# Optimization experiments

Hardware: AMD Instinct MI355X
Metric: run time of the kernel (lower is better)

## Reference

```python
import jax, jax.numpy as jnp
import numpy as np

L = 11
SF = 2
N, C, H, W = 8, 8, 256, 256


def _conv3(x, w, b):
    y = jax.lax.conv_general_dilated(x, w, (1, 1), ((1, 1), (1, 1)),
                                     dimension_numbers=('NCHW', 'OIHW', 'NCHW'))
    return y + b[None, :, None, None]


def _resblock(x, wa, ba, wb, bb):
    return _conv3(jax.nn.relu(_conv3(x, wa, ba)), wb, bb)


def _pronet(g, w1a, b1a, w1b, b1b, w2a, b2a, w2b, b2b, w3a, b3a, w3b, b3b,
            w4a, b4a, w4b, b4b, w5, b5):
    x1 = jax.nn.relu(g + 0.1 * _resblock(g, w1a, b1a, w1b, b1b))
    x2 = jax.nn.relu(x1 + 0.1 * _resblock(x1, w2a, b2a, w2b, b2b))
    x3 = jax.nn.relu(x2 + 0.1 * _resblock(x2, w3a, b3a, w3b, b3b))
    x4 = jax.nn.relu(x3 + 0.1 * _resblock(x3, w4a, b4a, w4b, b4b))
    return jax.nn.relu(g + 0.1 * _conv3(x4, w5, b5))


def _im2col(x, l, sf):
    # reflect-pad by (l-1)//2 then extract l x l patches with stride sf
    # -> [N, C, l*l, h*w], matching torch unfold's (c, kh, kw) channel order
    pad = (l - 1) // 2
    xp = jnp.pad(x, ((0, 0), (0, 0), (pad, pad), (pad, pad)), mode='reflect')
    n, c, hp, wp = xp.shape
    h = (hp - l) // sf + 1
    w = (wp - l) // sf + 1
    cols = [xp[:, :, i:i + (h - 1) * sf + 1:sf, j:j + (w - 1) * sf + 1:sf]
            for i in range(l) for j in range(l)]
    return jnp.stack(cols, axis=2).reshape(n, c, l * l, h * w), h, w


def setup_inputs() -> dict:
    key = jax.random.key(0)
    ks = jax.random.split(key, 22)
    h = (H - 1) // SF + 1
    inp = {
        'x': jax.random.normal(ks[0], (N, C, H, W), jnp.float32),
        'y': jax.random.normal(ks[1], (N, C, h, h), jnp.float32),
        'k': jax.random.uniform(ks[2], (N, C, L, L), jnp.float32),
        'sf': SF,
        'gamma': jnp.ones((), jnp.float32),
    }
    names = ['w1a', 'w1b', 'w2a', 'w2b', 'w3a', 'w3b', 'w4a', 'w4b', 'w5']
    for i, nm in enumerate(names):
        inp[nm] = 0.05 * jax.random.normal(ks[3 + i], (C, C, 3, 3), jnp.float32)
        inp['b' + nm[1:]] = 0.01 * jax.random.normal(ks[12 + i], (C,), jnp.float32)
    return inp


def reference(x, y, k, sf, gamma,
              w1a, b1a, w1b, b1b, w2a, b2a, w2b, b2b,
              w3a, b3a, w3b, b3b, w4a, b4a, w4b, b4b, w5, b5):
    n, c = x.shape[0], x.shape[1]
    l = k.shape[-1]
    x_col, h, w = _im2col(x, l, sf)                      # [N, C, l*l, h*w]
    kflat = k.reshape(n, c, l * l)
    # BatchBlur (grouped depthwise conv, groups=B*C) expressed as patch contraction
    blur = jnp.einsum('nckp,nck->ncp', x_col, kflat).reshape(n, c, h, w)
    # faithful torch .view: reinterpret [N,C,h,w] contiguous data as [N, h*w, C]
    R = (blur - y).reshape(n, h * w, c)
    # per-channel matmul loop fused into one batched contraction
    G = jnp.einsum('nckp,npc->nkc', x_col, R) / (h * w)  # [N, l*l, C]
    # faithful torch .view: reinterpret [N, l*l, C] as [N, C, l, l]
    G_K = k - (gamma / 10.0) * G.reshape(n, c, l, l)
    K = jax.nn.relu(_pronet(G_K, w1a, b1a, w1b, b1b, w2a, b2a, w2b, b2b,
                            w3a, b3a, w3b, b3b, w4a, b4a, w4b, b4b, w5, b5))
    return K / jnp.sum(K, axis=(2, 3), keepdims=True)
```

## Files before the change

kernel.cpp:

```cpp
#include <hip/hip_runtime.h>


__device__ __forceinline__ int refl(int m) {
    m = (m < 0) ? -m : m;
    return (m > 255) ? (510 - m) : m;
}

#define XPROW 272

__global__ __launch_bounds__(256) void pad_kernel(
        const float* __restrict__ x, float* __restrict__ xp) {
    int bid = blockIdx.x;
    int orig = (bid & 7) * 32 + (bid >> 3);
    int chunk = orig & 3;
    int nc = orig >> 2;
    int team = threadIdx.x >> 6;
    int lane = threadIdx.x & 63;
    const float* xb = x + nc * 65536;
    float* xpb = xp + nc * (256 * XPROW);
    for (int it = 0; it < 16; ++it) {
        int row = chunk * 64 + it * 4 + team;
        const float* src = xb + row * 256;
        float* dst = xpb + row * XPROW + 8;
        float4 v = reinterpret_cast<const float4*>(src)[lane];
        reinterpret_cast<float4*>(dst)[lane] = v;
        if (lane < 8) {
            dst[-1 - lane] = src[1 + lane];
        } else if (lane < 16) {
            int j = lane - 8;
            dst[256 + j] = src[254 - j];
        }
    }
}

__global__ __launch_bounds__(256) void blur_kernel(
        const float* __restrict__ xp, const float* __restrict__ y,
        const float* __restrict__ kk, float* __restrict__ E2) {
    __shared__ float kl[121];
    int bid = blockIdx.x;
    int orig = ((bid & 7) << 7) | (bid >> 3);
    int rowblk = orig & 15;
    int nc = orig >> 4;
    int t = threadIdx.x;
    if (t < 121) kl[t] = kk[nc * 121 + t];
    __syncthreads();
    int r = rowblk * 8 + (t >> 5);
    int ps0 = (t & 31) * 4;
    const float* xb = xp + nc * (256 * XPROW);
    float a0 = 0.f, a1 = 0.f, a2 = 0.f, a3 = 0.f;
    #pragma unroll
    for (int i = 0; i < 11; ++i) {
        int iy = refl(2 * r - 5 + i);
        const float4* row4 = reinterpret_cast<const float4*>(xb + iy * XPROW + 2 * ps0);
        float w[24];
        #pragma unroll
        for (int q = 0; q < 6; ++q) {
            float4 v = row4[q];
            w[4 * q] = v.x; w[4 * q + 1] = v.y; w[4 * q + 2] = v.z; w[4 * q + 3] = v.w;
        }
        #pragma unroll
        for (int j = 0; j < 11; ++j) {
            float kv = kl[i * 11 + j];
            a0 = fmaf(w[j + 3], kv, a0);
            a1 = fmaf(w[j + 5], kv, a1);
            a2 = fmaf(w[j + 7], kv, a2);
            a3 = fmaf(w[j + 9], kv, a3);
        }
    }
    int n = nc >> 3;
    int o = nc * 16384 + r * 128 + ps0;
    float4 yv = *reinterpret_cast<const float4*>(y + o);
    float e[4] = {a0 - yv.x, a1 - yv.y, a2 - yv.z, a3 - yv.w};
    int qn = o - n * 131072;
    int p = qn >> 3;
    int cbase = qn & 7;
    float* eb = E2 + n * 131072 + p;
    #pragma unroll
    for (int qq = 0; qq < 4; ++qq)
        eb[(cbase + qq) * 16384] = e[qq];
}

__global__ __launch_bounds__(256) void grad_kernel(
        const float* __restrict__ xp, const float* __restrict__ E2,
        float* __restrict__ G) {
    int bid = blockIdx.x;
    int orig = (bid & 7) * 88 + (bid >> 3);
    int ki = orig % 11;
    int nc = orig / 11;
    int n = nc >> 3, c = nc & 7;
    const float* xb = xp + nc * (256 * XPROW);
    const float* Eb = E2 + n * 131072 + c * 16384;
    int t = threadIdx.x;
    int ps0 = (t & 31) * 4;
    int pr0 = t >> 5;
    float acc[11];
    #pragma unroll
    for (int j = 0; j < 11; ++j) acc[j] = 0.f;
    for (int it = 0; it < 16; ++it) {
        int pr = pr0 + (it << 3);
        int iy = refl(ki + 2 * pr - 5);
        float4 ev = *reinterpret_cast<const float4*>(Eb + pr * 128 + ps0);
        const float4* row4 = reinterpret_cast<const float4*>(xb + iy * XPROW + 2 * ps0);
        float w[24];
        #pragma unroll
        for (int q = 0; q < 6; ++q) {
            float4 v = row4[q];
            w[4 * q] = v.x; w[4 * q + 1] = v.y; w[4 * q + 2] = v.z; w[4 * q + 3] = v.w;
        }
        #pragma unroll
        for (int j = 0; j < 11; ++j) {
            float v = acc[j];
            v = fmaf(w[j + 3], ev.x, v);
            v = fmaf(w[j + 5], ev.y, v);
            v = fmaf(w[j + 7], ev.z, v);
            v = fmaf(w[j + 9], ev.w, v);
            acc[j] = v;
        }
    }
    __shared__ float part[4][11];
    int lane = t & 63, wid = t >> 6;
    #pragma unroll
    for (int j = 0; j < 11; ++j) {
        float v = acc[j];
        #pragma unroll
        for (int off = 32; off > 0; off >>= 1)
            v += __shfl_down(v, off, 64);
        if (lane == 0) part[wid][j] = v;
    }
    __syncthreads();
    if (t < 11) {
        float s = part[0][t] + part[1][t] + part[2][t] + part[3][t];
        G[n * 968 + (ki * 11 + t) * 8 + c] = s * (1.0f / 16384.0f);
    }
}

__global__ __launch_bounds__(256) void blur_kernel_ref(
        const float* __restrict__ x, const float* __restrict__ y,
        const float* __restrict__ kk, float* __restrict__ E2) {
    __shared__ float kl[121];
    int bid = blockIdx.x;
    int rowblk = bid & 15;
    int nc = bid >> 4;
    int t = threadIdx.x;
    if (t < 121) kl[t] = kk[nc * 121 + t];
    __syncthreads();
    int r = rowblk * 8 + (t >> 5);
    int ps0 = (t & 31) * 4;
    const float* xb = x + nc * 65536;
    float a0 = 0.f, a1 = 0.f, a2 = 0.f, a3 = 0.f;
    int cb = 2 * ps0 - 5;
    #pragma unroll
    for (int i = 0; i < 11; ++i) {
        int iy = refl(2 * r - 5 + i);
        const float* row = xb + iy * 256;
        float c[17];
        #pragma unroll
        for (int u = 0; u < 17; ++u) c[u] = row[refl(cb + u)];
        #pragma unroll
        for (int j = 0; j < 11; ++j) {
            float kv = kl[i * 11 + j];
            a0 = fmaf(c[j], kv, a0);
            a1 = fmaf(c[j + 2], kv, a1);
            a2 = fmaf(c[j + 4], kv, a2);
            a3 = fmaf(c[j + 6], kv, a3);
        }
    }
    int n = nc >> 3;
    int o = nc * 16384 + r * 128 + ps0;
    float4 yv = *reinterpret_cast<const float4*>(y + o);
    float e[4] = {a0 - yv.x, a1 - yv.y, a2 - yv.z, a3 - yv.w};
    int qn = o - n * 131072;
    int p = qn >> 3;
    int cbase = qn & 7;
    float* eb = E2 + n * 131072 + p;
    #pragma unroll
    for (int qq = 0; qq < 4; ++qq)
        eb[(cbase + qq) * 16384] = e[qq];
}

__global__ __launch_bounds__(256) void grad_kernel_ref(
        const float* __restrict__ x, const float* __restrict__ E2,
        float* __restrict__ G) {
    int bid = blockIdx.x;
    int ki = bid % 11;
    int nc = bid / 11;
    int n = nc >> 3, c = nc & 7;
    const float* xb = x + nc * 65536;
    const float* Eb = E2 + n * 131072 + c * 16384;
    int t = threadIdx.x;
    int ps0 = (t & 31) * 4;
    int pr0 = t >> 5;
    int cb = 2 * ps0 - 5;
    float acc[11];
    #pragma unroll
    for (int j = 0; j < 11; ++j) acc[j] = 0.f;
    for (int it = 0; it < 16; ++it) {
        int pr = pr0 + (it << 3);
        int iy = refl(ki + 2 * pr - 5);
        const float* row = xb + iy * 256;
        float cbuf[17];
        #pragma unroll
        for (int u = 0; u < 17; ++u) cbuf[u] = row[refl(cb + u)];
        float4 ev = *reinterpret_cast<const float4*>(Eb + pr * 128 + ps0);
        #pragma unroll
        for (int j = 0; j < 11; ++j) {
            float v = acc[j];
            v = fmaf(cbuf[j], ev.x, v);
            v = fmaf(cbuf[j + 2], ev.y, v);
            v = fmaf(cbuf[j + 4], ev.z, v);
            v = fmaf(cbuf[j + 6], ev.w, v);
            acc[j] = v;
        }
    }
    __shared__ float part[4][11];
    int lane = t & 63, wid = t >> 6;
    #pragma unroll
    for (int j = 0; j < 11; ++j) {
        float v = acc[j];
        #pragma unroll
        for (int off = 32; off > 0; off >>= 1)
            v += __shfl_down(v, off, 64);
        if (lane == 0) part[wid][j] = v;
    }
    __syncthreads();
    if (t < 11) {
        float s = part[0][t] + part[1][t] + part[2][t] + part[3][t];
        G[n * 968 + (ki * 11 + t) * 8 + c] = s * (1.0f / 16384.0f);
    }
}

struct PArgs {
    const float* W[9];
    const float* B[9];
    const float* k;
    const float* gamma;
    const float* G;
    float* out;
};

#define PLSTRIDE 20
#define WSTRIDE 12

__global__ __launch_bounds__(704) void pronet_kernel(PArgs pa) {
    __shared__ __align__(16) float P0[8 * 13 * PLSTRIDE];
    __shared__ __align__(16) float P1[8 * 13 * PLSTRIDE];
    __shared__ float G2[968];
    __shared__ float F[968];
    __shared__ __align__(16) float red[7 * 88 * WSTRIDE];
    __shared__ __align__(16) float wts[9 * 64 * WSTRIDE];
    __shared__ float bs[9 * 8];
    __shared__ float rowsum[88];
    __shared__ float inv[8];

    int n = blockIdx.x;
    int t = threadIdx.x;

    #pragma unroll
    for (int widx = 0; widx < 9; ++widx) {
        if (t < 144) {
            float4 v = reinterpret_cast<const float4*>(pa.W[widx])[t];
            float vv[4] = {v.x, v.y, v.z, v.w};
            #pragma unroll
            for (int q2 = 0; q2 < 4; ++q2) {
                int g = 4 * t + q2;
                int oc = g / 9, q = g - oc * 9;
                wts[(widx * 64 + oc) * WSTRIDE + q] = vv[q2];
            }
        } else if (t >= 640 && t < 648) {
            bs[widx * 8 + (t - 640)] = pa.B[widx][t - 640];
        }
    }
    for (int i = t; i < 8 * 13 * PLSTRIDE; i += 704) { P0[i] = 0.f; P1[i] = 0.f; }
    __syncthreads();

    float gm = pa.gamma[0] * 0.1f;
    for (int o = t; o < 968; o += 704) {
        float v = pa.k[n * 968 + o] - gm * pa.G[n * 968 + o];
        G2[o] = v;
        int co = o / 121, rem = o - co * 121;
        int yy = rem / 11, xx = rem - yy * 11;
        P0[(co * 13 + yy + 1) * PLSTRIDE + xx + 1] = v;
    }

    int oct = t / 88;
    int id = t - oct * 88;
    int co = id / 11, yy = id - co * 11;
    int ci = oct;

    auto do_conv = [&](const float* Pin, int widx, int mode) {
        __syncthreads();
        float acc[12];
        {
            #pragma unroll
            for (int xx = 0; xx < 12; ++xx) acc[xx] = 0.f;
            const float4* wp4 = reinterpret_cast<const float4*>(
                &wts[(widx * 64 + co * 8 + ci) * WSTRIDE]);
            float4 w0 = wp4[0], w1 = wp4[1], w2 = wp4[2];
            float wv[9] = {w0.x, w0.y, w0.z, w0.w, w1.x, w1.y, w1.z, w1.w, w2.x};
            float r[3][13];
            #pragma unroll
            for (int dy = 0; dy < 3; ++dy) {
                const float* row = Pin + (ci * 13 + yy + dy) * PLSTRIDE;
                float4 a = *reinterpret_cast<const float4*>(row);
                float4 b = *reinterpret_cast<const float4*>(row + 4);
                float4 c = *reinterpret_cast<const float4*>(row + 8);
                r[dy][0] = a.x;  r[dy][1] = a.y;  r[dy][2]  = a.z;  r[dy][3]  = a.w;
                r[dy][4] = b.x;  r[dy][5] = b.y;  r[dy][6]  = b.z;  r[dy][7]  = b.w;
                r[dy][8] = c.x;  r[dy][9] = c.y;  r[dy][10] = c.z;  r[dy][11] = c.w;
                r[dy][12] = row[12];
            }
            #pragma unroll
            for (int xx = 0; xx < 11; ++xx) {
                float v = acc[xx];
                v = fmaf(r[0][xx],     wv[0], v);
                v = fmaf(r[0][xx + 1], wv[1], v);
                v = fmaf(r[0][xx + 2], wv[2], v);
                v = fmaf(r[1][xx],     wv[3], v);
                v = fmaf(r[1][xx + 1], wv[4], v);
                v = fmaf(r[1][xx + 2], wv[5], v);
                v = fmaf(r[2][xx],     wv[6], v);
                v = fmaf(r[2][xx + 1], wv[7], v);
                v = fmaf(r[2][xx + 2], wv[8], v);
                acc[xx] = v;
            }
            if (oct != 0) {
                float4* rp = reinterpret_cast<float4*>(
                    &red[((oct - 1) * 88 + id) * WSTRIDE]);
                rp[0] = make_float4(acc[0], acc[1], acc[2],  acc[3]);
                rp[1] = make_float4(acc[4], acc[5], acc[6],  acc[7]);
                rp[2] = make_float4(acc[8], acc[9], acc[10], acc[11]);
            }
        }
        __syncthreads();
        if (oct == 0) {
            float b = bs[widx * 8 + co];
            float oth[12];
            #pragma unroll
            for (int pq = 0; pq < 7; ++pq) {
                const float4* rp = reinterpret_cast<const float4*>(
                    &red[(pq * 88 + id) * WSTRIDE]);
                float4 v0 = rp[0], v1 = rp[1], v2 = rp[2];
                if (pq == 0) {
                    oth[0] = v0.x; oth[1] = v0.y; oth[2]  = v0.z; oth[3]  = v0.w;
                    oth[4] = v1.x; oth[5] = v1.y; oth[6]  = v1.z; oth[7]  = v1.w;
                    oth[8] = v2.x; oth[9] = v2.y; oth[10] = v2.z; oth[11] = v2.w;
                } else {
                    oth[0] += v0.x; oth[1] += v0.y; oth[2]  += v0.z; oth[3]  += v0.w;
                    oth[4] += v1.x; oth[5] += v1.y; oth[6]  += v1.z; oth[7]  += v1.w;
                    oth[8] += v2.x; oth[9] += v2.y; oth[10] += v2.z; oth[11] += v2.w;
                }
            }
            #pragma unroll
            for (int xx = 0; xx < 11; ++xx) {
                float v = acc[xx] + oth[xx] + b;
                int pidx = (co * 13 + yy + 1) * PLSTRIDE + xx + 1;
                if (mode == 0) {
                    P1[pidx] = fmaxf(v, 0.f);
                } else if (mode == 1) {
                    float p = P0[pidx];
                    P0[pidx] = fmaxf(fmaf(0.1f, v, p), 0.f);
                } else {
                    int fo = co * 121 + yy * 11 + xx;
                    F[fo] = fmaxf(fmaf(0.1f, v, G2[fo]), 0.f);
                }
            }
        }
    };

    #pragma unroll
    for (int rb = 0; rb < 4; ++rb) {
        do_conv(P0, 2 * rb, 0);
        do_conv(P1, 2 * rb + 1, 1);
    }
    do_conv(P0, 8, 2);
    __syncthreads();

    if (t < 88) {
        int tco = t / 11, tyy = t - tco * 11;
        float s = 0.f;
        #pragma unroll
        for (int xx = 0; xx < 11; ++xx) s += F[tco * 121 + tyy * 11 + xx];
        rowsum[t] = s;
    }
    __syncthreads();
    if (t < 8) {
        float s = 0.f;
        #pragma unroll
        for (int j = 0; j < 11; ++j) s += rowsum[t * 11 + j];
        inv[t] = 1.f / s;
    }
    __syncthreads();
    for (int o = t; o < 968; o += 704)
        pa.out[n * 968 + o] = F[o] * inv[o / 121];
}

extern "C" void kernel_launch(void* const* d_in, const int* in_sizes, int n_in,
                              void* d_out, int out_size, void* d_ws, size_t ws_size,
                              hipStream_t stream) {
    const float* x = (const float*)d_in[0];
    const float* y = (const float*)d_in[1];
    const float* k = (const float*)d_in[2];
    const float* gamma = (const float*)d_in[4];

    const size_t xpad_fl = (size_t)64 * 256 * XPROW;
    const size_t e2_fl = (size_t)8 * 131072;
    const size_t need = (xpad_fl + e2_fl + 7744) * sizeof(float);

    float* G;
    if (ws_size >= need) {
        float* xpad = (float*)d_ws;
        float* E2 = xpad + xpad_fl;
        G = E2 + e2_fl;
        pad_kernel<<<256, 256, 0, stream>>>(x, xpad);
        blur_kernel<<<1024, 256, 0, stream>>>(xpad, y, k, E2);
        grad_kernel<<<704, 256, 0, stream>>>(xpad, E2, G);
    } else {
        float* E2 = (float*)d_ws;
        G = E2 + e2_fl;
        blur_kernel_ref<<<1024, 256, 0, stream>>>(x, y, k, E2);
        grad_kernel_ref<<<704, 256, 0, stream>>>(x, E2, G);
    }

    PArgs pa;
    for (int i = 0; i < 9; ++i) {
        pa.W[i] = (const float*)d_in[5 + 2 * i];
        pa.B[i] = (const float*)d_in[6 + 2 * i];
    }
    pa.k = k;
    pa.gamma = gamma;
    pa.G = G;
    pa.out = (float*)d_out;
    pronet_kernel<<<8, 704, 0, stream>>>(pa);
}
```

Measured before the change: 168.1 us.

## Fuse blur and gradient kernels, keeping residual in LDS and reducing with atomics

Merges the blur and gradient kernels into one. Each block computes its tile of the blur residual into shared memory, then immediately uses it to accumulate gradient contributions, finished with a warp reduction and global atomicAdd. This removes the E2 round-trip through global memory and one kernel launch. G is now zeroed inside the pad kernel, and the 1/16384 scale moves into pronet. The cost is heavy atomic traffic on a small G array and a different floating-point summation order.

```diff
diff --git a/kernel.cpp b/kernel.cpp
--- a/kernel.cpp
+++ b/kernel.cpp
@@ -7,10 +7,15 @@
 }
 
 #define XPROW 272
+#define ESTRIDE 130
 
 __global__ __launch_bounds__(256) void pad_kernel(
-        const float* __restrict__ x, float* __restrict__ xp) {
+        const float* __restrict__ x, float* __restrict__ xp,
+        float* __restrict__ G) {
     int bid = blockIdx.x;
+    if (bid < 8) {
+        for (int i = threadIdx.x; i < 968; i += 256) G[bid * 968 + i] = 0.f;
+    }
     int orig = (bid & 7) * 32 + (bid >> 3);
     int chunk = orig & 3;
     int nc = orig >> 2;
@@ -33,104 +38,95 @@
     }
 }
 
-__global__ __launch_bounds__(256) void blur_kernel(
+__global__ __launch_bounds__(256) void fused_kernel(
         const float* __restrict__ xp, const float* __restrict__ y,
-        const float* __restrict__ kk, float* __restrict__ E2) {
+        const float* __restrict__ kk, float* __restrict__ G) {
     __shared__ float kl[121];
+    __shared__ float El[8 * ESTRIDE];
     int bid = blockIdx.x;
     int orig = ((bid & 7) << 7) | (bid >> 3);
     int rowblk = orig & 15;
-    int nc = orig >> 4;
+    int chat = (orig >> 4) & 7;
+    int n = orig >> 7;
+    int nc = n * 8 + chat;
     int t = threadIdx.x;
     if (t < 121) kl[t] = kk[nc * 121 + t];
     __syncthreads();
-    int r = rowblk * 8 + (t >> 5);
-    int ps0 = (t & 31) * 4;
-    const float* xb = xp + nc * (256 * XPROW);
-    float a0 = 0.f, a1 = 0.f, a2 = 0.f, a3 = 0.f;
-    #pragma unroll
-    for (int i = 0; i < 11; ++i) {
-        int iy = refl(2 * r - 5 + i);
-        const float4* row4 = reinterpret_cast<const float4*>(xb + iy * XPROW + 2 * ps0);
+
+    int cg = t & 31;
+    int ps0 = cg * 4;
+
+    {
+        const float* xb = xp + nc * (256 * XPROW);
+        int rg = t >> 5;
+        int r = rowblk * 8 + rg;
+        float a0 = 0.f, a1 = 0.f, a2 = 0.f, a3 = 0.f;
+        #pragma unroll
+        for (int i = 0; i < 11; ++i) {
+            int iy = refl(2 * r - 5 + i);
+            const float4* row4 =
+                reinterpret_cast<const float4*>(xb + iy * XPROW + 2 * ps0);
+            float w[24];
+            #pragma unroll
+            for (int q = 0; q < 6; ++q) {
+                float4 v = row4[q];
+                w[4 * q] = v.x; w[4 * q + 1] = v.y;
+                w[4 * q + 2] = v.z; w[4 * q + 3] = v.w;
+            }
+            #pragma unroll
+            for (int j = 0; j < 11; ++j) {
+                float kv = kl[i * 11 + j];
+                a0 = fmaf(w[j + 3], kv, a0);
+                a1 = fmaf(w[j + 5], kv, a1);
+                a2 = fmaf(w[j + 7], kv, a2);
+                a3 = fmaf(w[j + 9], kv, a3);
+            }
+        }
+        float4 yv = *reinterpret_cast<const float4*>(
+            y + nc * 16384 + r * 128 + ps0);
+        float* ep = &El[rg * ESTRIDE + ps0];
+        *reinterpret_cast<float2*>(ep)     = make_float2(a0 - yv.x, a1 - yv.y);
+        *reinterpret_cast<float2*>(ep + 2) = make_float2(a2 - yv.z, a3 - yv.w);
+    }
+    __syncthreads();
+
+    int cp = t >> 5;
+    int prs = chat * 16 + rowblk;
+    const float* xb = xp + (n * 8 + cp) * (256 * XPROW);
+    int ebase = (cg >> 2) * ESTRIDE + (cg & 3) * 32 + cp;
+    float e0 = El[ebase], e1 = El[ebase + 8],
+          e2 = El[ebase + 16], e3 = El[ebase + 24];
+    float* gb = G + n * 968 + cp;
+    #pragma unroll 1
+    for (int ki = 0; ki < 11; ++ki) {
+        int iy = refl(ki + 2 * prs - 5);
+        const float4* row4 =
+            reinterpret_cast<const float4*>(xb + iy * XPROW + 2 * ps0);
         float w[24];
         #pragma unroll
         for (int q = 0; q < 6; ++q) {
             float4 v = row4[q];
-            w[4 * q] = v.x; w[4 * q + 1] = v.y; w[4 * q + 2] = v.z; w[4 * q + 3] = v.w;
-        }
-        #pragma unroll
-        for (int j = 0; j < 11; ++j) {
-            float kv = kl[i * 11 + j];
-            a0 = fmaf(w[j + 3], kv, a0);
-            a1 = fmaf(w[j + 5], kv, a1);
-            a2 = fmaf(w[j + 7], kv, a2);
-            a3 = fmaf(w[j + 9], kv, a3);
-        }
-    }
-    int n = nc >> 3;
-    int o = nc * 16384 + r * 128 + ps0;
-    float4 yv = *reinterpret_cast<const float4*>(y + o);
-    float e[4] = {a0 - yv.x, a1 - yv.y, a2 - yv.z, a3 - yv.w};
-    int qn = o - n * 131072;
-    int p = qn >> 3;
-    int cbase = qn & 7;
-    float* eb = E2 + n * 131072 + p;
-    #pragma unroll
-    for (int qq = 0; qq < 4; ++qq)
-        eb[(cbase + qq) * 16384] = e[qq];
-}
-
-__global__ __launch_bounds__(256) void grad_kernel(
-        const float* __restrict__ xp, const float* __restrict__ E2,
-        float* __restrict__ G) {
-    int bid = blockIdx.x;
-    int orig = (bid & 7) * 88 + (bid >> 3);
-    int ki = orig % 11;
-    int nc = orig / 11;
-    int n = nc >> 3, c = nc & 7;
-    const float* xb = xp + nc * (256 * XPROW);
-    const float* Eb = E2 + n * 131072 + c * 16384;
-    int t = threadIdx.x;
-    int ps0 = (t & 31) * 4;
-    int pr0 = t >> 5;
-    float acc[11];
-    #pragma unroll
-    for (int j = 0; j < 11; ++j) acc[j] = 0.f;
-    for (int it = 0; it < 16; ++it) {
-        int pr = pr0 + (it << 3);
-        int iy = refl(ki + 2 * pr - 5);
-        float4 ev = *reinterpret_cast<const float4*>(Eb + pr * 128 + ps0);
-        const float4* row4 = reinterpret_cast<const float4*>(xb + iy * XPROW + 2 * ps0);
-        float w[24];
-        #pragma unroll
-        for (int q = 0; q < 6; ++q) {
-            float4 v = row4[q];
-            w[4 * q] = v.x; w[4 * q + 1] = v.y; w[4 * q + 2] = v.z; w[4 * q + 3] = v.w;
-        }
-        #pragma unroll
-        for (int j = 0; j < 11; ++j) {
-            float v = acc[j];
-            v = fmaf(w[j + 3], ev.x, v);
-            v = fmaf(w[j + 5], ev.y, v);
-            v = fmaf(w[j + 7], ev.z, v);
-            v = fmaf(w[j + 9], ev.w, v);
-            acc[j] = v;
-        }
-    }
-    __shared__ float part[4][11];
-    int lane = t & 63, wid = t >> 6;
-    #pragma unroll
-    for (int j = 0; j < 11; ++j) {
-        float v = acc[j];
-        #pragma unroll
-        for (int off = 32; off > 0; off >>= 1)
-            v += __shfl_down(v, off, 64);
-        if (lane == 0) part[wid][j] = v;
-    }
-    __syncthreads();
-    if (t < 11) {
-        float s = part[0][t] + part[1][t] + part[2][t] + part[3][t];
-        G[n * 968 + (ki * 11 + t) * 8 + c] = s * (1.0f / 16384.0f);
+            w[4 * q] = v.x; w[4 * q + 1] = v.y;
+            w[4 * q + 2] = v.z; w[4 * q + 3] = v.w;
+        }
+        float acc[11];
+        #pragma unroll
+        for (int kj = 0; kj < 11; ++kj) {
+            float v = w[kj + 3] * e0;
+            v = fmaf(w[kj + 5], e1, v);
+            v = fmaf(w[kj + 7], e2, v);
+            v = fmaf(w[kj + 9], e3, v);
+            acc[kj] = v;
+        }
+        #pragma unroll
+        for (int kj = 0; kj < 11; ++kj) {
+            float v = acc[kj];
+            #pragma unroll
+            for (int off = 16; off > 0; off >>= 1)
+                v += __shfl_down(v, off, 32);
+            if ((t & 31) == 0)
+                atomicAdd(&gb[(ki * 11 + kj) * 8], v);
+        }
     }
 }
 
@@ -225,7 +221,7 @@
     __syncthreads();
     if (t < 11) {
         float s = part[0][t] + part[1][t] + part[2][t] + part[3][t];
-        G[n * 968 + (ki * 11 + t) * 8 + c] = s * (1.0f / 16384.0f);
+        G[n * 968 + (ki * 11 + t) * 8 + c] = s;
     }
 }
 
@@ -273,7 +269,7 @@
     for (int i = t; i < 8 * 13 * PLSTRIDE; i += 704) { P0[i] = 0.f; P1[i] = 0.f; }
     __syncthreads();
 
-    float gm = pa.gamma[0] * 0.1f;
+    float gm = pa.gamma[0] * 0.1f * (1.0f / 16384.0f);
     for (int o = t; o < 968; o += 704) {
         float v = pa.k[n * 968 + o] - gm * pa.G[n * 968 + o];
         G2[o] = v;
@@ -404,16 +400,14 @@
 
     const size_t xpad_fl = (size_t)64 * 256 * XPROW;
     const size_t e2_fl = (size_t)8 * 131072;
-    const size_t need = (xpad_fl + e2_fl + 7744) * sizeof(float);
+    const size_t need_main = (xpad_fl + 7744) * sizeof(float);
 
     float* G;
-    if (ws_size >= need) {
+    if (ws_size >= need_main) {
         float* xpad = (float*)d_ws;
-        float* E2 = xpad + xpad_fl;
-        G = E2 + e2_fl;
-        pad_kernel<<<256, 256, 0, stream>>>(x, xpad);
-        blur_kernel<<<1024, 256, 0, stream>>>(xpad, y, k, E2);
-        grad_kernel<<<704, 256, 0, stream>>>(xpad, E2, G);
+        G = xpad + xpad_fl;
+        pad_kernel<<<256, 256, 0, stream>>>(x, xpad, G);
+        fused_kernel<<<1024, 256, 0, stream>>>(xpad, y, k, G);
     } else {
         float* E2 = (float*)d_ws;
         G = E2 + e2_fl;
```

New measurement: 249.5 us. 1.48x slower.

## Split blur and grad kernels into smaller blocks with partial-sum gradient reduction

Applied to the files above, without the earlier changes.

Blur blocks are halved to 128 threads covering 4 rows, doubling the grid. The grad kernel is split across 4 row quarters per (n,c,ki), and each block writes an unscaled partial sum. The pronet kernel then adds the partials and applies the 1/16384 scale. This aims to improve occupancy and load balance on the many CUs, at the cost of more blocks, extra partial-buffer traffic and a small serial reduction in pronet.

```diff
diff --git a/kernel.cpp b/kernel.cpp
--- a/kernel.cpp
+++ b/kernel.cpp
@@ -33,18 +33,18 @@
     }
 }
 
-__global__ __launch_bounds__(256) void blur_kernel(
+__global__ __launch_bounds__(128) void blur_kernel(
         const float* __restrict__ xp, const float* __restrict__ y,
         const float* __restrict__ kk, float* __restrict__ E2) {
     __shared__ float kl[121];
     int bid = blockIdx.x;
-    int orig = ((bid & 7) << 7) | (bid >> 3);
-    int rowblk = orig & 15;
-    int nc = orig >> 4;
+    int orig = ((bid & 7) << 8) | (bid >> 3);
+    int rb = orig & 31;
+    int nc = orig >> 5;
     int t = threadIdx.x;
     if (t < 121) kl[t] = kk[nc * 121 + t];
     __syncthreads();
-    int r = rowblk * 8 + (t >> 5);
+    int r = rb * 4 + (t >> 5);
     int ps0 = (t & 31) * 4;
     const float* xb = xp + nc * (256 * XPROW);
     float a0 = 0.f, a1 = 0.f, a2 = 0.f, a3 = 0.f;
@@ -56,7 +56,8 @@
         #pragma unroll
         for (int q = 0; q < 6; ++q) {
             float4 v = row4[q];
-            w[4 * q] = v.x; w[4 * q + 1] = v.y; w[4 * q + 2] = v.z; w[4 * q + 3] = v.w;
+            w[4 * q] = v.x; w[4 * q + 1] = v.y;
+            w[4 * q + 2] = v.z; w[4 * q + 3] = v.w;
         }
         #pragma unroll
         for (int j = 0; j < 11; ++j) {
@@ -80,13 +81,15 @@
         eb[(cbase + qq) * 16384] = e[qq];
 }
 
-__global__ __launch_bounds__(256) void grad_kernel(
+__global__ __launch_bounds__(128) void grad_kernel(
         const float* __restrict__ xp, const float* __restrict__ E2,
-        float* __restrict__ G) {
+        float* __restrict__ Gp) {
     int bid = blockIdx.x;
-    int orig = (bid & 7) * 88 + (bid >> 3);
-    int ki = orig % 11;
-    int nc = orig / 11;
+    int orig = (bid & 7) * 352 + (bid >> 3);
+    int qt = orig & 3;
+    int kinc = orig >> 2;
+    int ki = kinc % 11;
+    int nc = kinc / 11;
     int n = nc >> 3, c = nc & 7;
     const float* xb = xp + nc * (256 * XPROW);
     const float* Eb = E2 + n * 131072 + c * 16384;
@@ -96,8 +99,9 @@
     float acc[11];
     #pragma unroll
     for (int j = 0; j < 11; ++j) acc[j] = 0.f;
-    for (int it = 0; it < 16; ++it) {
-        int pr = pr0 + (it << 3);
+    #pragma unroll
+    for (int it = 0; it < 8; ++it) {
+        int pr = qt * 32 + pr0 + (it << 2);
         int iy = refl(ki + 2 * pr - 5);
         float4 ev = *reinterpret_cast<const float4*>(Eb + pr * 128 + ps0);
         const float4* row4 = reinterpret_cast<const float4*>(xb + iy * XPROW + 2 * ps0);
@@ -105,7 +109,8 @@
         #pragma unroll
         for (int q = 0; q < 6; ++q) {
             float4 v = row4[q];
-            w[4 * q] = v.x; w[4 * q + 1] = v.y; w[4 * q + 2] = v.z; w[4 * q + 3] = v.w;
+            w[4 * q] = v.x; w[4 * q + 1] = v.y;
+            w[4 * q + 2] = v.z; w[4 * q + 3] = v.w;
         }
         #pragma unroll
         for (int j = 0; j < 11; ++j) {
@@ -117,7 +122,7 @@
             acc[j] = v;
         }
     }
-    __shared__ float part[4][11];
+    __shared__ float part[2][11];
     int lane = t & 63, wid = t >> 6;
     #pragma unroll
     for (int j = 0; j < 11; ++j) {
@@ -129,8 +134,8 @@
     }
     __syncthreads();
     if (t < 11) {
-        float s = part[0][t] + part[1][t] + part[2][t] + part[3][t];
-        G[n * 968 + (ki * 11 + t) * 8 + c] = s * (1.0f / 16384.0f);
+        float s = part[0][t] + part[1][t];
+        Gp[qt * 7744 + n * 968 + (ki * 11 + t) * 8 + c] = s;
     }
 }
 
@@ -180,7 +185,7 @@
 
 __global__ __launch_bounds__(256) void grad_kernel_ref(
         const float* __restrict__ x, const float* __restrict__ E2,
-        float* __restrict__ G) {
+        float* __restrict__ Gp) {
     int bid = blockIdx.x;
     int ki = bid % 11;
     int nc = bid / 11;
@@ -225,7 +230,7 @@
     __syncthreads();
     if (t < 11) {
         float s = part[0][t] + part[1][t] + part[2][t] + part[3][t];
-        G[n * 968 + (ki * 11 + t) * 8 + c] = s * (1.0f / 16384.0f);
+        Gp[n * 968 + (ki * 11 + t) * 8 + c] = s;
     }
 }
 
@@ -241,7 +246,7 @@
 #define PLSTRIDE 20
 #define WSTRIDE 12
 
-__global__ __launch_bounds__(704) void pronet_kernel(PArgs pa) {
+__global__ __launch_bounds__(704) void pronet_kernel(PArgs pa, int npart) {
     __shared__ __align__(16) float P0[8 * 13 * PLSTRIDE];
     __shared__ __align__(16) float P1[8 * 13 * PLSTRIDE];
     __shared__ float G2[968];
@@ -273,9 +278,12 @@
     for (int i = t; i < 8 * 13 * PLSTRIDE; i += 704) { P0[i] = 0.f; P1[i] = 0.f; }
     __syncthreads();
 
-    float gm = pa.gamma[0] * 0.1f;
+    float gm = pa.gamma[0] * 0.1f * (1.0f / 16384.0f);
     for (int o = t; o < 968; o += 704) {
-        float v = pa.k[n * 968 + o] - gm * pa.G[n * 968 + o];
+        float s = 0.f;
+        for (int p = 0; p < npart; ++p)
+            s += pa.G[p * 7744 + n * 968 + o];
+        float v = pa.k[n * 968 + o] - gm * s;
         G2[o] = v;
         int co = o / 121, rem = o - co * 121;
         int yy = rem / 11, xx = rem - yy * 11;
@@ -404,21 +412,24 @@
 
     const size_t xpad_fl = (size_t)64 * 256 * XPROW;
     const size_t e2_fl = (size_t)8 * 131072;
-    const size_t need = (xpad_fl + e2_fl + 7744) * sizeof(float);
-
-    float* G;
-    if (ws_size >= need) {
+    const size_t need_main = (xpad_fl + e2_fl + 4 * 7744) * sizeof(float);
+
+    float* Gp;
+    int npart;
+    if (ws_size >= need_main) {
         float* xpad = (float*)d_ws;
         float* E2 = xpad + xpad_fl;
-        G = E2 + e2_fl;
+        Gp = E2 + e2_fl;
+        npart = 4;
         pad_kernel<<<256, 256, 0, stream>>>(x, xpad);
-        blur_kernel<<<1024, 256, 0, stream>>>(xpad, y, k, E2);
-        grad_kernel<<<704, 256, 0, stream>>>(xpad, E2, G);
+        blur_kernel<<<2048, 128, 0, stream>>>(xpad, y, k, E2);
+        grad_kernel<<<2816, 128, 0, stream>>>(xpad, E2, Gp);
     } else {
         float* E2 = (float*)d_ws;
-        G = E2 + e2_fl;
+        Gp = E2 + e2_fl;
+        npart = 1;
         blur_kernel_ref<<<1024, 256, 0, stream>>>(x, y, k, E2);
-        grad_kernel_ref<<<704, 256, 0, stream>>>(x, E2, G);
+        grad_kernel_ref<<<704, 256, 0, stream>>>(x, E2, Gp);
     }
 
     PArgs pa;
@@ -428,7 +439,7 @@
     }
     pa.k = k;
     pa.gamma = gamma;
-    pa.G = G;
+    pa.G = Gp;
     pa.out = (float*)d_out;
-    pronet_kernel<<<8, 704, 0, stream>>>(pa);
-}
+    pronet_kernel<<<8, 704, 0, stream>>>(pa, npart);
+}
```

New measurement: 173.1 us. +3.0%, slower.

## Fuse pad, blur and grad kernels into one cooperative kernel with grid syncs

Applied to the files above, without the earlier changes.

Merges the three pre-pronet kernels (reflect-pad, blur residual, gradient contraction) into a single cooperative launch of 1024 blocks, separated by grid-wide barriers. The goal is to remove two kernel launch gaps and tail effects between dependent stages. In exchange it takes on cooperative-launch overhead and grid.sync costs, and it requires all 1024 blocks to be co-resident (hence launch_bounds 256,4). The grad phase idles 5 of every 16 blocks.

```diff
diff --git a/kernel.cpp b/kernel.cpp
--- a/kernel.cpp
+++ b/kernel.cpp
@@ -1,4 +1,7 @@
 #include <hip/hip_runtime.h>
+#include <hip/hip_cooperative_groups.h>
+
+namespace cg = cooperative_groups;
 
 
 __device__ __forceinline__ int refl(int m) {
@@ -8,129 +11,129 @@
 
 #define XPROW 272
 
-__global__ __launch_bounds__(256) void pad_kernel(
-        const float* __restrict__ x, float* __restrict__ xp) {
-    int bid = blockIdx.x;
-    int orig = (bid & 7) * 32 + (bid >> 3);
-    int chunk = orig & 3;
-    int nc = orig >> 2;
-    int team = threadIdx.x >> 6;
-    int lane = threadIdx.x & 63;
-    const float* xb = x + nc * 65536;
-    float* xpb = xp + nc * (256 * XPROW);
-    for (int it = 0; it < 16; ++it) {
-        int row = chunk * 64 + it * 4 + team;
-        const float* src = xb + row * 256;
-        float* dst = xpb + row * XPROW + 8;
-        float4 v = reinterpret_cast<const float4*>(src)[lane];
-        reinterpret_cast<float4*>(dst)[lane] = v;
-        if (lane < 8) {
-            dst[-1 - lane] = src[1 + lane];
-        } else if (lane < 16) {
-            int j = lane - 8;
-            dst[256 + j] = src[254 - j];
-        }
-    }
-}
-
-__global__ __launch_bounds__(256) void blur_kernel(
-        const float* __restrict__ xp, const float* __restrict__ y,
-        const float* __restrict__ kk, float* __restrict__ E2) {
+__global__ __launch_bounds__(256, 4) void mega_kernel(
+        const float* __restrict__ x, const float* __restrict__ y,
+        const float* __restrict__ kk, float* __restrict__ xp,
+        float* __restrict__ E2, float* __restrict__ G) {
+    cg::grid_group grid = cg::this_grid();
     __shared__ float kl[121];
+    __shared__ float part[4][11];
+
     int bid = blockIdx.x;
     int orig = ((bid & 7) << 7) | (bid >> 3);
-    int rowblk = orig & 15;
+    int sub = orig & 15;
     int nc = orig >> 4;
+    int n = nc >> 3, c = nc & 7;
     int t = threadIdx.x;
-    if (t < 121) kl[t] = kk[nc * 121 + t];
-    __syncthreads();
-    int r = rowblk * 8 + (t >> 5);
-    int ps0 = (t & 31) * 4;
-    const float* xb = xp + nc * (256 * XPROW);
-    float a0 = 0.f, a1 = 0.f, a2 = 0.f, a3 = 0.f;
-    #pragma unroll
-    for (int i = 0; i < 11; ++i) {
-        int iy = refl(2 * r - 5 + i);
-        const float4* row4 = reinterpret_cast<const float4*>(xb + iy * XPROW + 2 * ps0);
-        float w[24];
-        #pragma unroll
-        for (int q = 0; q < 6; ++q) {
-            float4 v = row4[q];
-            w[4 * q] = v.x; w[4 * q + 1] = v.y; w[4 * q + 2] = v.z; w[4 * q + 3] = v.w;
-        }
-        #pragma unroll
-        for (int j = 0; j < 11; ++j) {
-            float kv = kl[i * 11 + j];
-            a0 = fmaf(w[j + 3], kv, a0);
-            a1 = fmaf(w[j + 5], kv, a1);
-            a2 = fmaf(w[j + 7], kv, a2);
-            a3 = fmaf(w[j + 9], kv, a3);
-        }
-    }
-    int n = nc >> 3;
-    int o = nc * 16384 + r * 128 + ps0;
-    float4 yv = *reinterpret_cast<const float4*>(y + o);
-    float e[4] = {a0 - yv.x, a1 - yv.y, a2 - yv.z, a3 - yv.w};
-    int qn = o - n * 131072;
-    int p = qn >> 3;
-    int cbase = qn & 7;
-    float* eb = E2 + n * 131072 + p;
-    #pragma unroll
-    for (int qq = 0; qq < 4; ++qq)
-        eb[(cbase + qq) * 16384] = e[qq];
-}
-
-__global__ __launch_bounds__(256) void grad_kernel(
-        const float* __restrict__ xp, const float* __restrict__ E2,
-        float* __restrict__ G) {
-    int bid = blockIdx.x;
-    int orig = (bid & 7) * 88 + (bid >> 3);
-    int ki = orig % 11;
-    int nc = orig / 11;
-    int n = nc >> 3, c = nc & 7;
-    const float* xb = xp + nc * (256 * XPROW);
-    const float* Eb = E2 + n * 131072 + c * 16384;
-    int t = threadIdx.x;
-    int ps0 = (t & 31) * 4;
-    int pr0 = t >> 5;
-    float acc[11];
-    #pragma unroll
-    for (int j = 0; j < 11; ++j) acc[j] = 0.f;
-    for (int it = 0; it < 16; ++it) {
-        int pr = pr0 + (it << 3);
-        int iy = refl(ki + 2 * pr - 5);
-        float4 ev = *reinterpret_cast<const float4*>(Eb + pr * 128 + ps0);
-        const float4* row4 = reinterpret_cast<const float4*>(xb + iy * XPROW + 2 * ps0);
-        float w[24];
-        #pragma unroll
-        for (int q = 0; q < 6; ++q) {
-            float4 v = row4[q];
-            w[4 * q] = v.x; w[4 * q + 1] = v.y; w[4 * q + 2] = v.z; w[4 * q + 3] = v.w;
-        }
+
+    {
+        int team = t >> 6;
+        int lane = t & 63;
+        const float* xb = x + nc * 65536;
+        float* xpb = xp + nc * (256 * XPROW);
+        #pragma unroll
+        for (int it = 0; it < 4; ++it) {
+            int row = 16 * sub + it * 4 + team;
+            const float* src = xb + row * 256;
+            float* dst = xpb + row * XPROW + 8;
+            float4 v = reinterpret_cast<const float4*>(src)[lane];
+            reinterpret_cast<float4*>(dst)[lane] = v;
+            if (lane < 8) {
+                dst[-1 - lane] = src[1 + lane];
+            } else if (lane < 16) {
+                int j = lane - 8;
+                dst[256 + j] = src[254 - j];
+            }
+        }
+        if (t < 121) kl[t] = kk[nc * 121 + t];
+    }
+    grid.sync();
+
+    {
+        int r = sub * 8 + (t >> 5);
+        int ps0 = (t & 31) * 4;
+        const float* xb = xp + nc * (256 * XPROW);
+        float a0 = 0.f, a1 = 0.f, a2 = 0.f, a3 = 0.f;
+        #pragma unroll
+        for (int i = 0; i < 11; ++i) {
+            int iy = refl(2 * r - 5 + i);
+            const float4* row4 =
+                reinterpret_cast<const float4*>(xb + iy * XPROW + 2 * ps0);
+            float w[24];
+            #pragma unroll
+            for (int q = 0; q < 6; ++q) {
+                float4 v = row4[q];
+                w[4 * q] = v.x; w[4 * q + 1] = v.y;
+                w[4 * q + 2] = v.z; w[4 * q + 3] = v.w;
+            }
+            #pragma unroll
+            for (int j = 0; j < 11; ++j) {
+                float kv = kl[i * 11 + j];
+                a0 = fmaf(w[j + 3], kv, a0);
+                a1 = fmaf(w[j + 5], kv, a1);
+                a2 = fmaf(w[j + 7], kv, a2);
+                a3 = fmaf(w[j + 9], kv, a3);
+            }
+        }
+        int o = nc * 16384 + r * 128 + ps0;
+        float4 yv = *reinterpret_cast<const float4*>(y + o);
+        float e[4] = {a0 - yv.x, a1 - yv.y, a2 - yv.z, a3 - yv.w};
+        int qn = o - n * 131072;
+        int p = qn >> 3;
+        int cbase = qn & 7;
+        float* eb = E2 + n * 131072 + p;
+        #pragma unroll
+        for (int qq = 0; qq < 4; ++qq)
+            eb[(cbase + qq) * 16384] = e[qq];
+    }
+    grid.sync();
+
+    if (sub < 11) {
+        int ki = sub;
+        const float* xb = xp + nc * (256 * XPROW);
+        const float* Eb = E2 + n * 131072 + c * 16384;
+        int ps0 = (t & 31) * 4;
+        int pr0 = t >> 5;
+        float acc[11];
+        #pragma unroll
+        for (int j = 0; j < 11; ++j) acc[j] = 0.f;
+        for (int it = 0; it < 16; ++it) {
+            int pr = pr0 + (it << 3);
+            int iy = refl(ki + 2 * pr - 5);
+            float4 ev = *reinterpret_cast<const float4*>(Eb + pr * 128 + ps0);
+            const float4* row4 =
+                reinterpret_cast<const float4*>(xb + iy * XPROW + 2 * ps0);
+            float w[24];
+            #pragma unroll
+            for (int q = 0; q < 6; ++q) {
+                float4 v = row4[q];
+                w[4 * q] = v.x; w[4 * q + 1] = v.y;
+                w[4 * q + 2] = v.z; w[4 * q + 3] = v.w;
+            }
+            #pragma unroll
+            for (int j = 0; j < 11; ++j) {
+                float v = acc[j];
+                v = fmaf(w[j + 3], ev.x, v);
+                v = fmaf(w[j + 5], ev.y, v);
+                v = fmaf(w[j + 7], ev.z, v);
+                v = fmaf(w[j + 9], ev.w, v);
+                acc[j] = v;
+            }
+        }
+        int lane = t & 63, wid = t >> 6;
         #pragma unroll
         for (int j = 0; j < 11; ++j) {
             float v = acc[j];
-            v = fmaf(w[j + 3], ev.x, v);
-            v = fmaf(w[j + 5], ev.y, v);
-            v = fmaf(w[j + 7], ev.z, v);
-            v = fmaf(w[j + 9], ev.w, v);
-            acc[j] = v;
-        }
-    }
-    __shared__ float part[4][11];
-    int lane = t & 63, wid = t >> 6;
-    #pragma unroll
-    for (int j = 0; j < 11; ++j) {
-        float v = acc[j];
-        #pragma unroll
-        for (int off = 32; off > 0; off >>= 1)
-            v += __shfl_down(v, off, 64);
-        if (lane == 0) part[wid][j] = v;
-    }
-    __syncthreads();
-    if (t < 11) {
-        float s = part[0][t] + part[1][t] + part[2][t] + part[3][t];
-        G[n * 968 + (ki * 11 + t) * 8 + c] = s * (1.0f / 16384.0f);
+            #pragma unroll
+            for (int off = 32; off > 0; off >>= 1)
+                v += __shfl_down(v, off, 64);
+            if (lane == 0) part[wid][j] = v;
+        }
+        __syncthreads();
+        if (t < 11) {
+            float s = part[0][t] + part[1][t] + part[2][t] + part[3][t];
+            G[n * 968 + (ki * 11 + t) * 8 + c] = s * (1.0f / 16384.0f);
+        }
     }
 }
 
@@ -153,16 +156,16 @@
     for (int i = 0; i < 11; ++i) {
         int iy = refl(2 * r - 5 + i);
         const float* row = xb + iy * 256;
-        float c[17];
-        #pragma unroll
-        for (int u = 0; u < 17; ++u) c[u] = row[refl(cb + u)];
+        float cbuf[17];
+        #pragma unroll
+        for (int u = 0; u < 17; ++u) cbuf[u] = row[refl(cb + u)];
         #pragma unroll
         for (int j = 0; j < 11; ++j) {
             float kv = kl[i * 11 + j];
-            a0 = fmaf(c[j], kv, a0);
-            a1 = fmaf(c[j + 2], kv, a1);
-            a2 = fmaf(c[j + 4], kv, a2);
-            a3 = fmaf(c[j + 6], kv, a3);
+            a0 = fmaf(cbuf[j], kv, a0);
+            a1 = fmaf(cbuf[j + 2], kv, a1);
+            a2 = fmaf(cbuf[j + 4], kv, a2);
+            a3 = fmaf(cbuf[j + 6], kv, a3);
         }
     }
     int n = nc >> 3;
@@ -411,9 +414,10 @@
         float* xpad = (float*)d_ws;
         float* E2 = xpad + xpad_fl;
         G = E2 + e2_fl;
-        pad_kernel<<<256, 256, 0, stream>>>(x, xpad);
-        blur_kernel<<<1024, 256, 0, stream>>>(xpad, y, k, E2);
-        grad_kernel<<<704, 256, 0, stream>>>(xpad, E2, G);
+        void* args[] = {(void*)&x, (void*)&y, (void*)&k,
+                        (void*)&xpad, (void*)&E2, (void*)&G};
+        hipLaunchCooperativeKernel((const void*)mega_kernel,
+                                   dim3(1024), dim3(256), args, 0, stream);
     } else {
         float* E2 = (float*)d_ws;
         G = E2 + e2_fl;
```

Measured after the change: 434.5 us. 2.58x slower.
